# Performance work log

Measured on AMD Instinct MI355X. Metric: run time of the kernel, lower is better.

## Reference

```python
import jax, jax.numpy as jnp
import numpy as np

B, H, NI, NT, D = 512, 1, 36, 50, 1024
NEG = -1e9
EPS = 1e-8

def setup_inputs() -> dict:
    key = jax.random.key(0)
    ks = jax.random.split(key, 12)
    s = 1.0 / np.sqrt(D)
    return {
        "imgE": jax.random.normal(ks[0], (B, H, NI, D), jnp.float32),
        "txtE": jax.random.normal(ks[1], (B, H, NT, D), jnp.float32),
        "x_mask": jax.random.randint(ks[2], (B, H, 1, NI), 0, 2).astype(bool),
        "y_mask": jax.random.randint(ks[3], (B, H, 1, NT), 0, 2).astype(bool),
        "W_img": jax.random.uniform(ks[4], (D, D), jnp.float32, -s, s),
        "b_img": jax.random.uniform(ks[5], (D,), jnp.float32, -s, s),
        "W_txt": jax.random.uniform(ks[6], (D, D), jnp.float32, -s, s),
        "b_txt": jax.random.uniform(ks[7], (D,), jnp.float32, -s, s),
        "W_img1": jax.random.uniform(ks[8], (D, D), jnp.float32, -s, s),
        "b_img1": jax.random.uniform(ks[9], (D,), jnp.float32, -s, s),
        "W_txt1": jax.random.uniform(ks[10], (D, D), jnp.float32, -s, s),
        "b_txt1": jax.random.uniform(ks[11], (D,), jnp.float32, -s, s),
    }

def reference(imgE, txtE, x_mask, y_mask,
              W_img, b_img, W_txt, b_txt, W_img1, b_img1, W_txt1, b_txt1):
    # projections
    x = jnp.einsum('bhnd,de->bhne', imgE, W_img) + b_img   # [B,H,NI,D]
    y = jnp.einsum('bhmd,de->bhme', txtE, W_txt) + b_txt   # [B,H,NT,D]
    # cosine-normalized attention scores [B,H,NI,NT]
    att = jnp.einsum('bhnd,bhmd->bhnm', x, y)
    wx = jnp.linalg.norm(x, axis=-1)[..., :, None]          # [B,H,NI,1]
    wy = jnp.linalg.norm(y, axis=-1)[..., None, :]          # [B,H,1,NT]
    att = att / jnp.maximum(wx * wy, EPS)
    # img <- txt direction
    att1 = jax.nn.softmax(jnp.where(y_mask, NEG, att), axis=-1)
    att_x = jnp.einsum('bhnm,bhmd->bhnd', att1, txtE)
    gate_x = jax.nn.sigmoid(att_x * imgE)
    fuse_x = jnp.einsum('bhnd,de->bhne', gate_x * att_x, W_img1) + b_img1
    img_out = fuse_x + imgE
    # txt <- img direction
    att2 = jax.nn.softmax(jnp.where(x_mask, NEG, jnp.swapaxes(att, 2, 3)), axis=-1)
    att_y = jnp.einsum('bhmn,bhnd->bhmd', att2, imgE)
    gate_y = jax.nn.sigmoid(att_y * txtE)
    fuse_y = jnp.einsum('bhmd,de->bhme', gate_y * att_y, W_txt1) + b_txt1
    txt_out = fuse_y + txtE
    return (img_out, txt_out)
```

## Files before the change

### kernel.cpp

```cpp
#include <hip/hip_runtime.h>

typedef unsigned short u16;
typedef unsigned int u32;
typedef __attribute__((ext_vector_type(8))) short sv8;
typedef __attribute__((ext_vector_type(4))) float fv4;

__device__ __forceinline__ u16 f2b(float f) {
  u32 u = __builtin_bit_cast(u32, f);
  u32 r = (u + 0x7fffu + ((u >> 16) & 1u)) >> 16;
  return (u16)r;
}
__device__ __forceinline__ float b2f(u16 h) {
  return __builtin_bit_cast(float, ((u32)h) << 16);
}
__device__ __forceinline__ void gld16(const void* g, void* l) {
  __builtin_amdgcn_global_load_lds(
      (const __attribute__((address_space(1))) u32*)g,
      (__attribute__((address_space(3))) u32*)l, 16, 0, 0);
}

__global__ __launch_bounds__(256) void cast_k(const float4* __restrict__ in,
                                              u16* __restrict__ out, int n4) {
  int i = blockIdx.x * 256 + threadIdx.x;
  const int stride = gridDim.x * 256;
  for (; i < n4; i += stride) {
    float4 v = in[i];
    u32 p0 = (u32)f2b(v.x) | ((u32)f2b(v.y) << 16);
    u32 p1 = (u32)f2b(v.z) | ((u32)f2b(v.w) << 16);
    uint2 o; o.x = p0; o.y = p1;
    ((uint2*)out)[i] = o;
  }
}

__global__ __launch_bounds__(256) void wtrans_k(const float* __restrict__ W0,
                                                const float* __restrict__ W1,
                                                const float* __restrict__ W2,
                                                const float* __restrict__ W3,
                                                u16* __restrict__ out) {
  const int z = blockIdx.z;
  const float* W = (z == 0) ? W0 : (z == 1) ? W1 : (z == 2) ? W2 : W3;
  u16* o = out + (size_t)z * 1048576;
  __shared__ float t[32][33];
  const int tid = threadIdx.x;
  const int r = tid >> 5, cc = tid & 31;
  const int d0 = blockIdx.x * 32, e0 = blockIdx.y * 32;
#pragma unroll
  for (int i = 0; i < 4; ++i)
    t[r + i * 8][cc] = W[(size_t)(d0 + r + i * 8) * 1024 + e0 + cc];
  __syncthreads();
#pragma unroll
  for (int i = 0; i < 4; ++i) {
    int row = r + i * 8;
    o[(size_t)(e0 + row) * 1024 + d0 + cc] = f2b(t[cc][row]);
  }
}

template <int MODE>
__global__ __launch_bounds__(256, 4) void gemm2_k(
    const u16* __restrict__ Aimg, const u16* __restrict__ Atxt,
    const u16* __restrict__ Wimg, const u16* __restrict__ Wtxt,
    const float* __restrict__ bii, const float* __restrict__ btt,
    const float* __restrict__ rii, const float* __restrict__ rtt,
    u16* __restrict__ obi, u16* __restrict__ obt,
    float* __restrict__ ofi, float* __restrict__ oft) {
  __shared__ __attribute__((aligned(16))) char smem[32768];
  const int tid = threadIdx.x;
  const int lane = tid & 63;
  const int w = tid >> 6;
  const int l15 = lane & 15, l4 = lane >> 4;
  const int lin = blockIdx.y * 8 + blockIdx.x;
  const int xcd = lin & 7, slot = lin >> 3;
  const int bcol0 = (slot & 7) * 128;
  const int prow = xcd + ((slot >> 3) << 3);

  const char* Ab; const char* Bb; const float* bias; const float* resid;
  u16* ob; float* of; int brow0;
  if (prow < 144) {
    brow0 = prow * 128;
    Ab = (const char*)Aimg + (size_t)brow0 * 2048;
    Bb = (const char*)Wimg + (size_t)bcol0 * 2048;
    bias = bii; resid = rii; ob = obi; of = ofi;
  } else {
    brow0 = (prow - 144) * 128;
    Ab = (const char*)Atxt + (size_t)brow0 * 2048;
    Bb = (const char*)Wtxt + (size_t)bcol0 * 2048;
    bias = btt; resid = rtt; ob = obt; of = oft;
  }
  const int wr = (w >> 1) * 64;
  const int wc = (w & 1) * 64;
  fv4 acc[4][4] = {};

  auto STAGE = [&](int bb, int k0) {
    char* base = smem + bb * 16384;
#pragma unroll
    for (int j = 0; j < 2; ++j) {
      int row = (w * 2 + j) * 16 + (lane >> 2);
      int g = (lane & 3) ^ ((row >> 1) & 3);
      gld16(Ab + (size_t)row * 2048 + k0 * 2 + g * 16,
            base + (w * 2 + j) * 1024 + lane * 16);
    }
#pragma unroll
    for (int j = 0; j < 2; ++j) {
      int row = (w * 2 + j) * 16 + (lane >> 2);
      int g = (lane & 3) ^ ((row >> 1) & 3);
      gld16(Bb + (size_t)row * 2048 + k0 * 2 + g * 16,
            base + 8192 + (w * 2 + j) * 1024 + lane * 16);
    }
  };

  STAGE(0, 0);
  for (int t = 0; t < 32; ++t) {
    const int cur = t & 1;
    if (t < 31) {
      STAGE(cur ^ 1, (t + 1) * 32);
      asm volatile("s_waitcnt vmcnt(4)" ::: "memory");
    } else {
      asm volatile("s_waitcnt vmcnt(0)" ::: "memory");
    }
    __builtin_amdgcn_s_barrier();
    __builtin_amdgcn_sched_barrier(0);
    const char* Tl = smem + cur * 16384;
    sv8 af[4], bf[4];
#pragma unroll
    for (int m = 0; m < 4; ++m) {
      int row = wr + m * 16 + l15;
      int c = l4 ^ ((row >> 1) & 3);
      af[m] = *(const sv8*)(Tl + row * 64 + c * 16);
    }
#pragma unroll
    for (int n = 0; n < 4; ++n) {
      int row = wc + n * 16 + l15;
      int c = l4 ^ ((row >> 1) & 3);
      bf[n] = *(const sv8*)(Tl + 8192 + row * 64 + c * 16);
    }
#pragma unroll
    for (int m = 0; m < 4; ++m)
#pragma unroll
      for (int n = 0; n < 4; ++n)
        acc[m][n] = __builtin_amdgcn_mfma_f32_16x16x32_bf16(af[m], bf[n], acc[m][n], 0, 0, 0);
    __builtin_amdgcn_sched_barrier(0);
    __builtin_amdgcn_s_barrier();
  }

  float bv[4];
#pragma unroll
  for (int n = 0; n < 4; ++n) bv[n] = bias[bcol0 + wc + n * 16 + l15];
#pragma unroll
  for (int m = 0; m < 4; ++m) {
#pragma unroll
    for (int j = 0; j < 4; ++j) {
      const int row = brow0 + wr + m * 16 + l4 * 4 + j;
#pragma unroll
      for (int n = 0; n < 4; ++n) {
        const int col = bcol0 + wc + n * 16 + l15;
        const size_t idx = (size_t)row * 1024 + col;
        float r = acc[m][n][j] + bv[n];
        if (MODE == 0) {
          ob[idx] = f2b(r);
        } else {
          float rv = __builtin_nontemporal_load(&resid[idx]);
          __builtin_nontemporal_store(r + rv, &of[idx]);
        }
      }
    }
  }
}

__global__ __launch_bounds__(512) void score_k(const u16* __restrict__ Xb,
                                               const u16* __restrict__ Yb,
                                               const void* __restrict__ xmask,
                                               const void* __restrict__ ymask,
                                               float* __restrict__ P1g,
                                               float* __restrict__ P2g) {
  __shared__ float attL[48 * 65];
  __shared__ float wxL[88];
  __shared__ unsigned char msk[88];
  const int b = blockIdx.x;
  const int tid = threadIdx.x;
  const int w = tid >> 6, lane = tid & 63;
  const int l15 = lane & 15, l4 = lane >> 4;

  u32 det = 0;
  {
    const u32* mm = (const u32*)xmask;
#pragma unroll
    for (int i = 0; i < 16; ++i) det |= mm[i * 4];
    det |= mm[1] | mm[2] | mm[3];
  }
  const bool m_i32 = (det <= 1u);
  if (tid < 36)
    msk[tid] = (unsigned char)(m_i32 ? (((const int*)xmask)[b * 36 + tid] != 0)
                                     : (((const unsigned char*)xmask)[b * 36 + tid] != 0));
  if (tid >= 64 && tid < 114) {
    int m = tid - 64;
    msk[36 + m] = (unsigned char)(m_i32 ? (((const int*)ymask)[b * 50 + m] != 0)
                                        : (((const unsigned char*)ymask)[b * 50 + m] != 0));
  }

  const u16* Xr = Xb + (size_t)b * 36864;
  const u16* Yr = Yb + (size_t)b * 51200;

  if (w < 4) {
#pragma unroll
    for (int sweep = 0; sweep < 3; ++sweep) {
      int r = sweep * 32 + (tid >> 3);
      int j = tid & 7;
      if (r < 86) {
        const u32* p = (const u32*)((r < 36) ? (Xr + r * 1024)
                                             : (Yr + (size_t)(r - 36) * 1024)) + j * 64;
        float s = 0.f;
#pragma unroll
        for (int i = 0; i < 16; ++i) {
          uint4 q = ((const uint4*)p)[i];
          u32 qq[4] = {q.x, q.y, q.z, q.w};
#pragma unroll
          for (int k2 = 0; k2 < 4; ++k2) {
            float lo = __builtin_bit_cast(float, qq[k2] << 16);
            float hi = __builtin_bit_cast(float, qq[k2] & 0xffff0000u);
            s = fmaf(lo, lo, fmaf(hi, hi, s));
          }
        }
        s += __shfl_xor(s, 1); s += __shfl_xor(s, 2); s += __shfl_xor(s, 4);
        if (j == 0) wxL[r] = sqrtf(s);
      }
    }
  } else {
    const int tn = w - 4;
    fv4 ac0 = {}, ac1 = {}, ac2 = {};
    const u16* Yp = Yr + (size_t)(tn * 16 + l15) * 1024 + l4 * 8;
    const u16* Xp = Xr + (size_t)l15 * 1024 + l4 * 8;
#pragma unroll 2
    for (int ks = 0; ks < 32; ++ks) {
      sv8 bf = *(const sv8*)(Yp + ks * 32);
      sv8 a0 = *(const sv8*)(Xp + ks * 32);
      sv8 a1 = *(const sv8*)(Xp + 16 * 1024 + ks * 32);
      sv8 a2 = *(const sv8*)(Xp + 32 * 1024 + ks * 32);
      ac0 = __builtin_amdgcn_mfma_f32_16x16x32_bf16(a0, bf, ac0, 0, 0, 0);
      ac1 = __builtin_amdgcn_mfma_f32_16x16x32_bf16(a1, bf, ac1, 0, 0, 0);
      ac2 = __builtin_amdgcn_mfma_f32_16x16x32_bf16(a2, bf, ac2, 0, 0, 0);
    }
    const int col = tn * 16 + l15;
#pragma unroll
    for (int j = 0; j < 4; ++j) {
      attL[(l4 * 4 + j) * 65 + col] = ac0[j];
      attL[(16 + l4 * 4 + j) * 65 + col] = ac1[j];
      attL[(32 + l4 * 4 + j) * 65 + col] = ac2[j];
    }
  }
  __syncthreads();

#pragma unroll
  for (int sweep = 0; sweep < 2; ++sweep) {
    int R = sweep * 64 + (tid >> 3);
    int j = tid & 7;
    if (R < 36) {
      float wxn = wxL[R];
      float sv[7];
#pragma unroll
      for (int i = 0; i < 7; ++i) {
        int m = j + i * 8;
        if (m < 50) {
          float den = fmaxf(wxn * wxL[36 + m], 1e-8f);
          float v = attL[R * 65 + m] / den;
          sv[i] = msk[36 + m] ? -1e9f : v;
        } else sv[i] = -3.4e38f;
      }
      float mx = sv[0];
#pragma unroll
      for (int i = 1; i < 7; ++i) mx = fmaxf(mx, sv[i]);
      mx = fmaxf(mx, __shfl_xor(mx, 1));
      mx = fmaxf(mx, __shfl_xor(mx, 2));
      mx = fmaxf(mx, __shfl_xor(mx, 4));
      float e[7], sum = 0.f;
#pragma unroll
      for (int i = 0; i < 7; ++i) {
        e[i] = (j + i * 8 < 50) ? __expf(sv[i] - mx) : 0.f;
        sum += e[i];
      }
      sum += __shfl_xor(sum, 1); sum += __shfl_xor(sum, 2); sum += __shfl_xor(sum, 4);
      float rs = 1.f / sum;
      float* dst = P1g + ((size_t)b * 36 + R) * 64;
#pragma unroll
      for (int i = 0; i < 7; ++i) {
        int m = j + i * 8;
        if (m < 50) dst[m] = e[i] * rs;
      }
    } else if (R < 86) {
      int m = R - 36;
      float wym = wxL[R];
      float sv[5];
#pragma unroll
      for (int i = 0; i < 5; ++i) {
        int n = j + i * 8;
        if (n < 36) {
          float den = fmaxf(wxL[n] * wym, 1e-8f);
          float v = attL[n * 65 + m] / den;
          sv[i] = msk[n] ? -1e9f : v;
        } else sv[i] = -3.4e38f;
      }
      float mx = sv[0];
#pragma unroll
      for (int i = 1; i < 5; ++i) mx = fmaxf(mx, sv[i]);
      mx = fmaxf(mx, __shfl_xor(mx, 1));
      mx = fmaxf(mx, __shfl_xor(mx, 2));
      mx = fmaxf(mx, __shfl_xor(mx, 4));
      float e[5], sum = 0.f;
#pragma unroll
      for (int i = 0; i < 5; ++i) {
        e[i] = (j + i * 8 < 36) ? __expf(sv[i] - mx) : 0.f;
        sum += e[i];
      }
      sum += __shfl_xor(sum, 1); sum += __shfl_xor(sum, 2); sum += __shfl_xor(sum, 4);
      float rs = 1.f / sum;
      float* dst = P2g + ((size_t)b * 50 + m) * 64;
#pragma unroll
      for (int i = 0; i < 5; ++i) {
        int n = j + i * 8;
        if (n < 36) dst[n] = e[i] * rs;
      }
    }
  }
}

__global__ __launch_bounds__(256) void pv_k(const float* __restrict__ P1g,
                                            const float* __restrict__ P2g,
                                            const u16* __restrict__ imgA,
                                            const u16* __restrict__ txtA,
                                            u16* __restrict__ gxw,
                                            u16* __restrict__ gyw) {
  __shared__ float ldsP1[36 * 64];
  __shared__ float ldsP2[50 * 64];
  const int b = blockIdx.x & 511;
  const int d = ((blockIdx.x >> 9) << 8) + threadIdx.x;
  const int tid = threadIdx.x;

  {
    const float4* s1 = (const float4*)(P1g + (size_t)b * 2304);
    float4* l1 = (float4*)ldsP1;
    for (int i = tid; i < 576; i += 256) l1[i] = s1[i];
    const float4* s2 = (const float4*)(P2g + (size_t)b * 3200);
    float4* l2 = (float4*)ldsP2;
    for (int i = tid; i < 800; i += 256) l2[i] = s2[i];
  }

  const u16* tp = txtA + (size_t)b * 51200 + d;
  const u16* ip = imgA + (size_t)b * 36864 + d;
  float tv[50], iv[36];
#pragma unroll
  for (int m = 0; m < 50; ++m) tv[m] = b2f(tp[(size_t)m * 1024]);
#pragma unroll
  for (int n = 0; n < 36; ++n) iv[n] = b2f(ip[(size_t)n * 1024]);
  __syncthreads();

  u16* gx = gxw + (size_t)b * 36864 + d;
#pragma unroll
  for (int n = 0; n < 36; ++n) {
    const float4* pr4 = (const float4*)(ldsP1 + n * 64);
    float4 a4 = {0.f, 0.f, 0.f, 0.f};
#pragma unroll
    for (int i = 0; i < 12; ++i) {
      float4 p = pr4[i];
      a4.x = fmaf(p.x, tv[4 * i + 0], a4.x);
      a4.y = fmaf(p.y, tv[4 * i + 1], a4.y);
      a4.z = fmaf(p.z, tv[4 * i + 2], a4.z);
      a4.w = fmaf(p.w, tv[4 * i + 3], a4.w);
    }
    float acc = (a4.x + a4.y) + (a4.z + a4.w);
    acc = fmaf(ldsP1[n * 64 + 48], tv[48], acc);
    acc = fmaf(ldsP1[n * 64 + 49], tv[49], acc);
    float t = acc * iv[n];
    float g = acc / (1.f + __expf(-t));
    gx[(size_t)n * 1024] = f2b(g);
  }
  u16* gy = gyw + (size_t)b * 51200 + d;
#pragma unroll
  for (int m = 0; m < 50; ++m) {
    const float4* pr4 = (const float4*)(ldsP2 + m * 64);
    float4 a4 = {0.f, 0.f, 0.f, 0.f};
#pragma unroll
    for (int i = 0; i < 9; ++i) {
      float4 p = pr4[i];
      a4.x = fmaf(p.x, iv[4 * i + 0], a4.x);
      a4.y = fmaf(p.y, iv[4 * i + 1], a4.y);
      a4.z = fmaf(p.z, iv[4 * i + 2], a4.z);
      a4.w = fmaf(p.w, iv[4 * i + 3], a4.w);
    }
    float acc = (a4.x + a4.y) + (a4.z + a4.w);
    float t = acc * tv[m];
    float g = acc / (1.f + __expf(-t));
    gy[(size_t)m * 1024] = f2b(g);
  }
}

extern "C" void kernel_launch(void* const* d_in, const int* in_sizes, int n_in,
                              void* d_out, int out_size, void* d_ws, size_t ws_size,
                              hipStream_t stream) {
  (void)in_sizes; (void)n_in; (void)out_size; (void)ws_size;
  const float* imgE = (const float*)d_in[0];
  const float* txtE = (const float*)d_in[1];
  const void* xmask = d_in[2];
  const void* ymask = d_in[3];
  const float* W_img  = (const float*)d_in[4];
  const float* b_img  = (const float*)d_in[5];
  const float* W_txt  = (const float*)d_in[6];
  const float* b_txt  = (const float*)d_in[7];
  const float* W_img1 = (const float*)d_in[8];
  const float* b_img1 = (const float*)d_in[9];
  const float* W_txt1 = (const float*)d_in[10];
  const float* b_txt1 = (const float*)d_in[11];
  float* out_img = (float*)d_out;
  float* out_txt = out_img + (size_t)18874368;

  char* ws = (char*)d_ws;
  u16* Wt   = (u16*)(ws);
  u16* imgA = (u16*)(ws + 8388608);
  u16* txtA = (u16*)(ws + 46137344);
  u16* Xb   = (u16*)(ws + 98566144);
  u16* Yb   = (u16*)(ws + 136314880);
  float* P1g = (float*)(ws + 188743680);
  float* P2g = (float*)(ws + 193462272);
  u16* gxw  = (u16*)(ws + 98566144);
  u16* gyw  = (u16*)(ws + 136314880);

  cast_k<<<2048, 256, 0, stream>>>((const float4*)imgE, imgA, 4718592);
  cast_k<<<2048, 256, 0, stream>>>((const float4*)txtE, txtA, 6553600);
  wtrans_k<<<dim3(32, 32, 4), 256, 0, stream>>>(W_img, W_txt, W_img1, W_txt1, Wt);
  gemm2_k<0><<<dim3(8, 344), 256, 0, stream>>>(
      imgA, txtA, Wt, Wt + 1048576, b_img, b_txt, nullptr, nullptr,
      Xb, Yb, nullptr, nullptr);
  score_k<<<512, 512, 0, stream>>>(Xb, Yb, xmask, ymask, P1g, P2g);
  pv_k<<<2048, 256, 0, stream>>>(P1g, P2g, imgA, txtA, gxw, gyw);
  gemm2_k<1><<<dim3(8, 344), 256, 0, stream>>>(
      gxw, gyw, Wt + 2097152, Wt + 3145728, b_img1, b_txt1, imgE, txtE,
      nullptr, nullptr, out_img, out_txt);
}
```

Measured before the change: 446.3 us.

## Triple-buffer GEMM K-loop and pack bf16 epilogue stores via lane shuffles

Moves the projection GEMM from double-buffered to triple-buffered LDS staging, so two K-tiles of global_load_lds are in flight while the current tile is computed. Shared memory grows to 48KB and the occupancy hint drops from 4 to 3 blocks per SM. The bf16 output epilogue now uses lane shuffles to pack two adjacent columns into one 32-bit store instead of writing individual 16-bit values. The cost is lower occupancy and extra shuffle instructions in the epilogue.

```diff
diff --git a/kernel.cpp b/kernel.cpp
--- a/kernel.cpp
+++ b/kernel.cpp
@@ -56,14 +56,14 @@
 }
 
 template <int MODE>
-__global__ __launch_bounds__(256, 4) void gemm2_k(
+__global__ __launch_bounds__(256, 3) void gemm2_k(
     const u16* __restrict__ Aimg, const u16* __restrict__ Atxt,
     const u16* __restrict__ Wimg, const u16* __restrict__ Wtxt,
     const float* __restrict__ bii, const float* __restrict__ btt,
     const float* __restrict__ rii, const float* __restrict__ rtt,
     u16* __restrict__ obi, u16* __restrict__ obt,
     float* __restrict__ ofi, float* __restrict__ oft) {
-  __shared__ __attribute__((aligned(16))) char smem[32768];
+  __shared__ __attribute__((aligned(16))) char smem[49152];
   const int tid = threadIdx.x;
   const int lane = tid & 63;
   const int w = tid >> 6;
@@ -108,18 +108,8 @@
     }
   };
 
-  STAGE(0, 0);
-  for (int t = 0; t < 32; ++t) {
-    const int cur = t & 1;
-    if (t < 31) {
-      STAGE(cur ^ 1, (t + 1) * 32);
-      asm volatile("s_waitcnt vmcnt(4)" ::: "memory");
-    } else {
-      asm volatile("s_waitcnt vmcnt(0)" ::: "memory");
-    }
-    __builtin_amdgcn_s_barrier();
-    __builtin_amdgcn_sched_barrier(0);
-    const char* Tl = smem + cur * 16384;
+  auto COMPUTE = [&](int bb) {
+    const char* Tl = smem + bb * 16384;
     sv8 af[4], bf[4];
 #pragma unroll
     for (int m = 0; m < 4; ++m) {
@@ -138,26 +128,67 @@
 #pragma unroll
       for (int n = 0; n < 4; ++n)
         acc[m][n] = __builtin_amdgcn_mfma_f32_16x16x32_bf16(af[m], bf[n], acc[m][n], 0, 0, 0);
+  };
+
+  STAGE(0, 0);
+  STAGE(1, 32);
+  int sb = 2, rb = 0;
+  for (int t = 0; t < 30; ++t) {
+    STAGE(sb, (t + 2) * 32);
+    sb = (sb == 2) ? 0 : sb + 1;
+    asm volatile("s_waitcnt vmcnt(8)" ::: "memory");
+    __builtin_amdgcn_s_barrier();
+    __builtin_amdgcn_sched_barrier(0);
+    COMPUTE(rb);
+    rb = (rb == 2) ? 0 : rb + 1;
     __builtin_amdgcn_sched_barrier(0);
     __builtin_amdgcn_s_barrier();
   }
+  asm volatile("s_waitcnt vmcnt(4)" ::: "memory");
+  __builtin_amdgcn_s_barrier();
+  COMPUTE(rb);
+  rb = (rb == 2) ? 0 : rb + 1;
+  asm volatile("s_waitcnt vmcnt(0)" ::: "memory");
+  __builtin_amdgcn_s_barrier();
+  COMPUTE(rb);
 
   float bv[4];
 #pragma unroll
   for (int n = 0; n < 4; ++n) bv[n] = bias[bcol0 + wc + n * 16 + l15];
-#pragma unroll
-  for (int m = 0; m < 4; ++m) {
-#pragma unroll
-    for (int j = 0; j < 4; ++j) {
-      const int row = brow0 + wr + m * 16 + l4 * 4 + j;
-#pragma unroll
-      for (int n = 0; n < 4; ++n) {
-        const int col = bcol0 + wc + n * 16 + l15;
-        const size_t idx = (size_t)row * 1024 + col;
-        float r = acc[m][n][j] + bv[n];
-        if (MODE == 0) {
-          ob[idx] = f2b(r);
-        } else {
+
+  if (MODE == 0) {
+#pragma unroll
+    for (int m = 0; m < 4; ++m) {
+#pragma unroll
+      for (int j = 0; j < 4; ++j) {
+        const int row = brow0 + wr + m * 16 + l4 * 4 + j;
+        float x0 = acc[m][0][j] + bv[0], x1 = acc[m][1][j] + bv[1];
+        float x2 = acc[m][2][j] + bv[2], x3 = acc[m][3][j] + bv[3];
+        const int sl0 = (lane & 48) + ((2 * l15) & 15);
+        const bool lo8 = (l15 < 8);
+#pragma unroll
+        for (int q = 0; q < 2; ++q) {
+          float xa = q ? x2 : x0, xb = q ? x3 : x1;
+          float a0 = __shfl(xa, sl0),     b0 = __shfl(xb, sl0);
+          float a1 = __shfl(xa, sl0 + 1), b1 = __shfl(xb, sl0 + 1);
+          float v0 = lo8 ? a0 : b0;
+          float v1 = lo8 ? a1 : b1;
+          u32 pk = (u32)f2b(v0) | ((u32)f2b(v1) << 16);
+          *(u32*)((char*)ob + (size_t)row * 2048 + (size_t)(bcol0 + wc + q * 32) * 2 + l15 * 4) = pk;
+        }
+      }
+    }
+  } else {
+#pragma unroll
+    for (int m = 0; m < 4; ++m) {
+#pragma unroll
+      for (int j = 0; j < 4; ++j) {
+        const int row = brow0 + wr + m * 16 + l4 * 4 + j;
+#pragma unroll
+        for (int n = 0; n < 4; ++n) {
+          const int col = bcol0 + wc + n * 16 + l15;
+          const size_t idx = (size_t)row * 1024 + col;
+          float r = acc[m][n][j] + bv[n];
           float rv = __builtin_nontemporal_load(&resid[idx]);
           __builtin_nontemporal_store(r + rv, &of[idx]);
         }
```

Measured after the change: 458.3 us. 1.03x slower.
